# Kernel tuning notes

Hardware: AMD Instinct MI355X
Metric: run time of the kernel (lower is better)

## Reference

```python
import jax, jax.numpy as jnp
import numpy as np
import math

SIZE = 64
NLAND = 8
N_ITER = 6


def setup_inputs() -> dict:
    key = jax.random.key(0)
    k1, k2, k3 = jax.random.split(key, 3)
    B, T, C = 4, 4096, 1024
    return {
        "q": jax.random.normal(k1, (B, T, C), dtype=jnp.float32),
        "k": jax.random.normal(k2, (B, T, C), dtype=jnp.float32),
        "v": jax.random.normal(k3, (B, T, C), dtype=jnp.float32),
    }


def _iterative_pinv(mat, n_iter=N_ITER):
    # Newton-Schulz iteration for pseudo-inverse of [..., m, m] kernel.
    m = mat.shape[-1]
    I = jnp.eye(m, dtype=mat.dtype)
    K = mat
    # NOTE: torch.max over the whole tensor (global scalar), faithful to source.
    V = (1.0 / jnp.max(jnp.sum(K, axis=-2))) * jnp.swapaxes(K, -1, -2)
    for _ in range(n_iter):
        KV = jnp.matmul(K, V)
        V = jnp.matmul(0.25 * V, 13.0 * I - jnp.matmul(KV, 15.0 * I - jnp.matmul(KV, 7.0 * I - KV)))
    return V


def reference(q, k, v):
    B, T, C = q.shape
    H = C // SIZE
    scale = 1.0 / math.sqrt(SIZE)
    # Faithful reshape (not transpose) as in the source module.
    qh = q.reshape(B, H, T, SIZE)
    kh = k.reshape(B, H, T, SIZE)
    vh = v.reshape(B, H, T, SIZE)
    # T % NLAND == 0 branch: landmark = segment mean over T//NLAND tokens.
    q_l = qh.reshape(B, H, NLAND, T // NLAND, SIZE).mean(axis=-2)  # [B,H,m,d]
    k_l = kh.reshape(B, H, NLAND, T // NLAND, SIZE).mean(axis=-2)
    kernel_1 = jax.nn.softmax(jnp.einsum('bhtd,bhmd->bhtm', qh, k_l) * scale, axis=-1)  # [B,H,T,m]
    kernel_2 = jax.nn.softmax(jnp.einsum('bhmd,bhnd->bhmn', q_l, k_l) * scale, axis=-1)  # [B,H,m,m]
    kernel_3 = jax.nn.softmax(jnp.einsum('bhmd,bhtd->bhmt', q_l, kh) * scale, axis=-1)  # [B,H,m,T]
    pinv = _iterative_pinv(kernel_2)  # [B,H,m,m]
    k3v = jnp.matmul(kernel_3, vh)    # [B,H,m,d]
    out = jnp.matmul(jnp.matmul(kernel_1, pinv), k3v)  # [B,H,T,d]
    return out.reshape(B, T, C)
```

## Files before the change

### kernel.cpp

```cpp
#include <hip/hip_runtime.h>
#include <math.h>

#define T_TOK 4096
#define DD 64
#define NHEADS 64
#define SEG 512
#define SCALE 0.125f

#define QL_OFF   0
#define KL_OFF   32768
#define K2_OFF   65536
#define CS_OFF   69632
#define KP_OFF   70144
#define PA_OFF   332288
#define PD_OFF   2429440
#define W2_OFF   2462208

#define WAVE_BAR() __builtin_amdgcn_wave_barrier()

__global__ __launch_bounds__(256) void qsum_kernel(
    const float* __restrict__ q, float* __restrict__ ws) {
  int tid = threadIdx.x;
  const float4* q4 = (const float4*)q + (size_t)blockIdx.x * 8192;
  float4 b[2][8];
#pragma unroll
  for (int i = 0; i < 8; ++i) b[0][i] = q4[i * 256 + tid];
  float4 a = make_float4(0.f, 0.f, 0.f, 0.f);
#pragma unroll
  for (int j = 0; j < 4; ++j) {
    if (j < 3) {
#pragma unroll
      for (int i = 0; i < 8; ++i)
        b[(j + 1) & 1][i] = q4[(j + 1) * 2048 + i * 256 + tid];
    }
#pragma unroll
    for (int i = 0; i < 8; ++i) {
      float4 x = b[j & 1][i];
      a.x += x.x; a.y += x.y; a.z += x.z; a.w += x.w;
    }
  }
  __shared__ float4 red[16][17];
  red[tid >> 4][tid & 15] = a;
  __syncthreads();
  if (tid < 16) {
    float4 s = make_float4(0.f, 0.f, 0.f, 0.f);
#pragma unroll
    for (int g = 0; g < 16; ++g) {
      float4 r = red[g][tid];
      s.x += r.x; s.y += r.y; s.z += r.z; s.w += r.w;
    }
    const float inv = 1.f / (float)SEG;
    s.x *= inv; s.y *= inv; s.z *= inv; s.w *= inv;
    ((float4*)(ws + QL_OFF))[blockIdx.x * 16 + tid] = s;
  }
}

__global__ __launch_bounds__(256) void kvpass_kernel(
    const float* __restrict__ k, const float* __restrict__ v,
    float* __restrict__ ws) {
  int tid = threadIdx.x;
  int w = tid >> 6, lane = tid & 63;
  int gw = blockIdx.x * 4 + w;
  int hb = gw >> 6;
  int t8 = lane >> 3, m8 = lane & 7;
  int r0 = lane >> 4;
  __shared__ float qls[8][68];
  __shared__ float pl_all[4][16][12];
  float (*pl)[12] = pl_all[w];

  if (tid < 128) {
    float4 x = ((const float4*)(ws + QL_OFF))[hb * 128 + tid];
    *(float4*)&qls[tid >> 4][(tid & 15) * 4] = x;
  }
  __syncthreads();

  size_t base4 = (size_t)gw * 1024;
  const float4* k4 = (const float4*)k + base4;
  const float4* v4 = (const float4*)v + base4;

  float4 acc0 = make_float4(0.f,0.f,0.f,0.f), acc1 = make_float4(0.f,0.f,0.f,0.f);
  float4 acc2 = make_float4(0.f,0.f,0.f,0.f), acc3 = make_float4(0.f,0.f,0.f,0.f);
  float4 acc4 = make_float4(0.f,0.f,0.f,0.f), acc5 = make_float4(0.f,0.f,0.f,0.f);
  float4 acc6 = make_float4(0.f,0.f,0.f,0.f), acc7 = make_float4(0.f,0.f,0.f,0.f);
  float4 ksa = make_float4(0.f,0.f,0.f,0.f), ksb = make_float4(0.f,0.f,0.f,0.f);
  float den0=0.f,den1=0.f,den2=0.f,den3=0.f,den4=0.f,den5=0.f,den6=0.f,den7=0.f;

#pragma unroll 1
  for (int tile = 0; tile < 4; ++tile) {
    float4 vb0 = v4[tile * 256 + lane];
    float4 vb1 = v4[tile * 256 + 64 + lane];
    float4 vb2 = v4[tile * 256 + 128 + lane];
    float4 vb3 = v4[tile * 256 + 192 + lane];
#pragma unroll
    for (int rep = 0; rep < 2; ++rep) {
      int t = rep * 8 + t8;
      float4 ka = k4[(tile * 16 + t) * 16 + m8 * 2];
      float4 kb = k4[(tile * 16 + t) * 16 + m8 * 2 + 1];
      ksa.x += ka.x; ksa.y += ka.y; ksa.z += ka.z; ksa.w += ka.w;
      ksb.x += kb.x; ksb.y += kb.y; ksb.z += kb.z; ksb.w += kb.w;
      float p[8];
#pragma unroll
      for (int j = 0; j < 8; ++j) {
        const float4* qr = (const float4*)&qls[j][m8 * 8];
        float4 qa = qr[0], qb = qr[1];
        float dp = ka.x*qa.x + ka.y*qa.y + ka.z*qa.z + ka.w*qa.w
                 + kb.x*qb.x + kb.y*qb.y + kb.z*qb.z + kb.w*qb.w;
        dp += __shfl_xor(dp, 1, 64);
        dp += __shfl_xor(dp, 2, 64);
        dp += __shfl_xor(dp, 4, 64);
        p[j] = __expf(dp * SCALE);
      }
      den0 += p[0]; den1 += p[1]; den2 += p[2]; den3 += p[3];
      den4 += p[4]; den5 += p[5]; den6 += p[6]; den7 += p[7];
      float4 lo = make_float4(p[0], p[1], p[2], p[3]);
      float4 hi = make_float4(p[4], p[5], p[6], p[7]);
      if (m8 == 0) *(float4*)&pl[t][0] = lo;
      if (m8 == 1) *(float4*)&pl[t][4] = hi;
    }
    WAVE_BAR();
#pragma unroll
    for (int i = 0; i < 4; ++i) {
      int t = i * 4 + r0;
      float4 plo = *(const float4*)&pl[t][0];
      float4 phi = *(const float4*)&pl[t][4];
      float4 vv = (i == 0) ? vb0 : (i == 1) ? vb1 : (i == 2) ? vb2 : vb3;
      acc0.x += plo.x*vv.x; acc0.y += plo.x*vv.y; acc0.z += plo.x*vv.z; acc0.w += plo.x*vv.w;
      acc1.x += plo.y*vv.x; acc1.y += plo.y*vv.y; acc1.z += plo.y*vv.z; acc1.w += plo.y*vv.w;
      acc2.x += plo.z*vv.x; acc2.y += plo.z*vv.y; acc2.z += plo.z*vv.z; acc2.w += plo.z*vv.w;
      acc3.x += plo.w*vv.x; acc3.y += plo.w*vv.y; acc3.z += plo.w*vv.z; acc3.w += plo.w*vv.w;
      acc4.x += phi.x*vv.x; acc4.y += phi.x*vv.y; acc4.z += phi.x*vv.z; acc4.w += phi.x*vv.w;
      acc5.x += phi.y*vv.x; acc5.y += phi.y*vv.y; acc5.z += phi.y*vv.z; acc5.w += phi.y*vv.w;
      acc6.x += phi.z*vv.x; acc6.y += phi.z*vv.y; acc6.z += phi.z*vv.z; acc6.w += phi.z*vv.w;
      acc7.x += phi.w*vv.x; acc7.y += phi.w*vv.y; acc7.z += phi.w*vv.z; acc7.w += phi.w*vv.w;
    }
    WAVE_BAR();
  }
  ksa.x += __shfl_xor(ksa.x, 8, 64); ksa.y += __shfl_xor(ksa.y, 8, 64);
  ksa.z += __shfl_xor(ksa.z, 8, 64); ksa.w += __shfl_xor(ksa.w, 8, 64);
  ksb.x += __shfl_xor(ksb.x, 8, 64); ksb.y += __shfl_xor(ksb.y, 8, 64);
  ksb.z += __shfl_xor(ksb.z, 8, 64); ksb.w += __shfl_xor(ksb.w, 8, 64);
  ksa.x += __shfl_xor(ksa.x, 16, 64); ksa.y += __shfl_xor(ksa.y, 16, 64);
  ksa.z += __shfl_xor(ksa.z, 16, 64); ksa.w += __shfl_xor(ksa.w, 16, 64);
  ksb.x += __shfl_xor(ksb.x, 16, 64); ksb.y += __shfl_xor(ksb.y, 16, 64);
  ksb.z += __shfl_xor(ksb.z, 16, 64); ksb.w += __shfl_xor(ksb.w, 16, 64);
  ksa.x += __shfl_xor(ksa.x, 32, 64); ksa.y += __shfl_xor(ksa.y, 32, 64);
  ksa.z += __shfl_xor(ksa.z, 32, 64); ksa.w += __shfl_xor(ksa.w, 32, 64);
  ksb.x += __shfl_xor(ksb.x, 32, 64); ksb.y += __shfl_xor(ksb.y, 32, 64);
  ksb.z += __shfl_xor(ksb.z, 32, 64); ksb.w += __shfl_xor(ksb.w, 32, 64);
  if (lane < 8) {
    ((float4*)(ws + KP_OFF))[gw * 16 + lane * 2] = ksa;
    ((float4*)(ws + KP_OFF))[gw * 16 + lane * 2 + 1] = ksb;
  }
  den0 += __shfl_xor(den0, 8, 64); den1 += __shfl_xor(den1, 8, 64);
  den2 += __shfl_xor(den2, 8, 64); den3 += __shfl_xor(den3, 8, 64);
  den4 += __shfl_xor(den4, 8, 64); den5 += __shfl_xor(den5, 8, 64);
  den6 += __shfl_xor(den6, 8, 64); den7 += __shfl_xor(den7, 8, 64);
  den0 += __shfl_xor(den0, 16, 64); den1 += __shfl_xor(den1, 16, 64);
  den2 += __shfl_xor(den2, 16, 64); den3 += __shfl_xor(den3, 16, 64);
  den4 += __shfl_xor(den4, 16, 64); den5 += __shfl_xor(den5, 16, 64);
  den6 += __shfl_xor(den6, 16, 64); den7 += __shfl_xor(den7, 16, 64);
  den0 += __shfl_xor(den0, 32, 64); den1 += __shfl_xor(den1, 32, 64);
  den2 += __shfl_xor(den2, 32, 64); den3 += __shfl_xor(den3, 32, 64);
  den4 += __shfl_xor(den4, 32, 64); den5 += __shfl_xor(den5, 32, 64);
  den6 += __shfl_xor(den6, 32, 64); den7 += __shfl_xor(den7, 32, 64);
  if (lane == 0) {
    *(float4*)&ws[PD_OFF + (size_t)gw * 8] = make_float4(den0, den1, den2, den3);
    *(float4*)&ws[PD_OFF + (size_t)gw * 8 + 4] = make_float4(den4, den5, den6, den7);
  }
#define ACC_RED(A) \
  A.x += __shfl_xor(A.x, 16, 64); A.y += __shfl_xor(A.y, 16, 64); \
  A.z += __shfl_xor(A.z, 16, 64); A.w += __shfl_xor(A.w, 16, 64); \
  A.x += __shfl_xor(A.x, 32, 64); A.y += __shfl_xor(A.y, 32, 64); \
  A.z += __shfl_xor(A.z, 32, 64); A.w += __shfl_xor(A.w, 32, 64);
  ACC_RED(acc0) ACC_RED(acc1) ACC_RED(acc2) ACC_RED(acc3)
  ACC_RED(acc4) ACC_RED(acc5) ACC_RED(acc6) ACC_RED(acc7)
#undef ACC_RED
  if (lane < 16) {
    float4* pa = (float4*)(ws + PA_OFF) + (size_t)gw * 128;
    pa[0 * 16 + lane] = acc0;
    pa[1 * 16 + lane] = acc1;
    pa[2 * 16 + lane] = acc2;
    pa[3 * 16 + lane] = acc3;
    pa[4 * 16 + lane] = acc4;
    pa[5 * 16 + lane] = acc5;
    pa[6 * 16 + lane] = acc6;
    pa[7 * 16 + lane] = acc7;
  }
}

__global__ __launch_bounds__(512) void prepk_kernel(float* __restrict__ ws) {
  int hb = blockIdx.x, tid = threadIdx.x;
  __shared__ float qls[8][68];
  __shared__ float kls[8][68];
  __shared__ float ee[8][9];
  int m = tid >> 6, d = tid & 63;
  float s = 0.f;
#pragma unroll
  for (int j = 0; j < 8; ++j)
    s += ws[KP_OFF + (size_t)(hb * 64 + m * 8 + j) * 64 + d];
  s *= (1.f / (float)SEG);
  kls[m][d] = s;
  ws[KL_OFF + hb * 512 + tid] = s;
  qls[m][d] = ws[QL_OFF + hb * 512 + tid];
  __syncthreads();
  if (tid < 64) {
    int i = tid >> 3, j = tid & 7;
    float dot = 0.f;
#pragma unroll
    for (int dd = 0; dd < 64; ++dd) dot += qls[i][dd] * kls[j][dd];
    ee[i][j] = __expf(dot * SCALE);
  }
  __syncthreads();
  if (tid < 64) {
    int i = tid >> 3, j = tid & 7;
    float ssum = 0.f;
#pragma unroll
    for (int jj = 0; jj < 8; ++jj) ssum += ee[i][jj];
    ws[K2_OFF + hb * 64 + tid] = ee[i][j] / ssum;
  }
  if (tid < 8) {
    float cs = 0.f;
    for (int ii = 0; ii < 8; ++ii) {
      float ssum = 0.f;
#pragma unroll
      for (int jj = 0; jj < 8; ++jj) ssum += ee[ii][jj];
      cs += ee[ii][tid] / ssum;
    }
    ws[CS_OFF + hb * 8 + tid] = cs;
  }
}

__global__ __launch_bounds__(512) void pinvw2_kernel(float* __restrict__ ws) {
  int hb = blockIdx.x, tid = threadIdx.x;
  __shared__ float k3vs[8][68];
  __shared__ float K[8][9], V[8][9], X[8][9], Y[8][9];
  __shared__ float smax;
  int m = tid >> 6, d = tid & 63;
  float s = 0.f, den = 0.f;
  for (int c = 0; c < 64; ++c) {
    s += ws[PA_OFF + (((size_t)hb * 64 + c) * 8 + m) * 64 + d];
    den += ws[PD_OFF + ((size_t)hb * 64 + c) * 8 + m];
  }
  k3vs[m][d] = s / den;
  if (tid < 64) {
    float mx = 0.f;
    for (int t = 0; t < 8; ++t) mx = fmaxf(mx, ws[CS_OFF + t * 64 + tid]);
    for (int off = 32; off; off >>= 1) mx = fmaxf(mx, __shfl_xor(mx, off, 64));
    if (tid == 0) smax = mx;
  }
  int i = (tid >> 3) & 7, j = tid & 7;
  if (tid < 64) K[i][j] = ws[K2_OFF + hb * 64 + tid];
  __syncthreads();
  if (tid < 64) V[i][j] = K[j][i] * (1.f / smax);
  __syncthreads();
  for (int it = 0; it < 6; ++it) {
    float x = 0.f;
    if (tid < 64) {
      for (int kk = 0; kk < 8; ++kk) x += K[i][kk] * V[kk][j];
      X[i][j] = x;
    }
    __syncthreads();
    float bm = 0.f;
    if (tid < 64) {
      for (int kk = 0; kk < 8; ++kk) bm += X[i][kk] * X[kk][j];
      bm = 7.f * x - bm;
      Y[i][j] = bm;
    }
    __syncthreads();
    float dm = 0.f;
    if (tid < 64) {
      for (int kk = 0; kk < 8; ++kk) dm += X[i][kk] * Y[kk][j];
      dm = 15.f * x - dm;
    }
    __syncthreads();
    if (tid < 64) Y[i][j] = dm;
    __syncthreads();
    float vd = 0.f;
    if (tid < 64) {
      for (int kk = 0; kk < 8; ++kk) vd += V[i][kk] * Y[kk][j];
      vd = 0.25f * (13.f * V[i][j] - vd);
    }
    __syncthreads();
    if (tid < 64) V[i][j] = vd;
    __syncthreads();
  }
  float o = 0.f;
#pragma unroll
  for (int jj = 0; jj < 8; ++jj) o += V[m][jj] * k3vs[jj][d];
  ws[W2_OFF + hb * 512 + tid] = o;
}

__global__ __launch_bounds__(256) void out_kernel(
    const float* __restrict__ q, float* __restrict__ out,
    const float* __restrict__ ws) {
  int tid = threadIdx.x;
  int w = tid >> 6, lane = tid & 63;
  int gw = blockIdx.x * 4 + w;
  int hb = gw >> 6;
  __shared__ float qt_all[4][16][68];
  __shared__ float pl_all[4][16][9];
  __shared__ float w2_all[4][8][68];
  float (*qt)[68] = qt_all[w];
  float (*pl)[9]  = pl_all[w];
  float (*w2)[68] = w2_all[w];

  int m = lane & 7;
  float4 klrow[16];
#pragma unroll
  for (int d4 = 0; d4 < 16; ++d4)
    klrow[d4] = ((const float4*)(ws + KL_OFF))[hb * 128 + m * 16 + d4];
#pragma unroll
  for (int i = 0; i < 2; ++i) {
    int f4 = i * 64 + lane;
    float4 y = ((const float4*)(ws + W2_OFF))[hb * 128 + f4];
    *(float4*)&w2[f4 >> 4][(f4 & 15) * 4] = y;
  }

  size_t base4 = (size_t)gw * 1024;
  const float4* q4 = (const float4*)q + base4;
  float4* o4 = (float4*)out + base4;
  float4 buf[2][4];
#pragma unroll
  for (int i = 0; i < 4; ++i) buf[0][i] = q4[i * 64 + lane];

#pragma unroll
  for (int tile = 0; tile < 4; ++tile) {
    int cur = tile & 1;
    if (tile < 3) {
#pragma unroll
      for (int i = 0; i < 4; ++i)
        buf[cur ^ 1][i] = q4[(tile + 1) * 256 + i * 64 + lane];
    }
#pragma unroll
    for (int i = 0; i < 4; ++i) {
      int f4 = i * 64 + lane;
      *(float4*)&qt[f4 >> 4][(f4 & 15) * 4] = buf[cur][i];
    }
    WAVE_BAR();
#pragma unroll
    for (int rep = 0; rep < 2; ++rep) {
      int t = rep * 8 + (lane >> 3);
      const float4* qr = (const float4*)&qt[t][0];
      float dot = 0.f;
#pragma unroll
      for (int d4 = 0; d4 < 16; ++d4) {
        float4 a = qr[d4];
        dot += a.x * klrow[d4].x + a.y * klrow[d4].y +
               a.z * klrow[d4].z + a.w * klrow[d4].w;
      }
      pl[t][m] = __expf(dot * SCALE);
    }
    WAVE_BAR();
#pragma unroll
    for (int i = 0; i < 4; ++i) {
      int t = i * 4 + (lane >> 4);
      int qd = lane & 15;
      float p0 = pl[t][0], p1 = pl[t][1], p2 = pl[t][2], p3 = pl[t][3];
      float p4 = pl[t][4], p5 = pl[t][5], p6 = pl[t][6], p7 = pl[t][7];
      float inv = 1.f / (p0 + p1 + p2 + p3 + p4 + p5 + p6 + p7);
      float4 acc = make_float4(0.f, 0.f, 0.f, 0.f);
      float pm[8] = {p0, p1, p2, p3, p4, p5, p6, p7};
#pragma unroll
      for (int m2 = 0; m2 < 8; ++m2) {
        float wgt = pm[m2] * inv;
        float4 wv = *(const float4*)&w2[m2][qd * 4];
        acc.x += wgt * wv.x; acc.y += wgt * wv.y;
        acc.z += wgt * wv.z; acc.w += wgt * wv.w;
      }
      o4[tile * 256 + i * 64 + lane] = acc;
    }
    WAVE_BAR();
  }
}

extern "C" void kernel_launch(void* const* d_in, const int* in_sizes, int n_in,
                              void* d_out, int out_size, void* d_ws, size_t ws_size,
                              hipStream_t stream) {
  const float* q = (const float*)d_in[0];
  const float* k = (const float*)d_in[1];
  const float* v = (const float*)d_in[2];
  float* out = (float*)d_out;
  float* ws = (float*)d_ws;

  qsum_kernel<<<512, 256, 0, stream>>>(q, ws);
  kvpass_kernel<<<1024, 256, 0, stream>>>(k, v, ws);
  prepk_kernel<<<NHEADS, 512, 0, stream>>>(ws);
  pinvw2_kernel<<<NHEADS, 512, 0, stream>>>(ws);
  out_kernel<<<1024, 256, 0, stream>>>(q, out, ws);
}
```

Baseline: 84.32 us.

## Halve per-wave token span in kvpass and combine wave pairs in LDS

The kvpass kernel now launches twice as many blocks, and each wave processes 32 tokens (2 tiles) instead of 64. This raises parallelism and memory-level concurrency across the GPU. Partial sums from pairs of waves are added in shared memory before being written, so the workspace layout and the number of partial records the downstream kernels read stay the same. The cost is an extra __syncthreads, some LDS traffic, and a per-wave epilogue of shuffle reductions that is now amortized over half as much work.

```diff
diff --git a/kernel.cpp b/kernel.cpp
--- a/kernel.cpp
+++ b/kernel.cpp
@@ -60,12 +60,13 @@
     float* __restrict__ ws) {
   int tid = threadIdx.x;
   int w = tid >> 6, lane = tid & 63;
-  int gw = blockIdx.x * 4 + w;
-  int hb = gw >> 6;
-  int t8 = lane >> 3, m8 = lane & 7;
-  int r0 = lane >> 4;
+  int hb = blockIdx.x >> 5;
+  int t8 = lane >> 3, m8 = lane & 7, r0 = lane >> 4;
   __shared__ float qls[8][68];
   __shared__ float pl_all[4][16][12];
+  __shared__ float4 accred[4][8][16];
+  __shared__ float4 ksred[4][16];
+  __shared__ float dens[4][8];
   float (*pl)[12] = pl_all[w];
 
   if (tid < 128) {
@@ -74,9 +75,9 @@
   }
   __syncthreads();
 
-  size_t base4 = (size_t)gw * 1024;
-  const float4* k4 = (const float4*)k + base4;
-  const float4* v4 = (const float4*)v + base4;
+  size_t tok0 = (size_t)blockIdx.x * 128 + (size_t)w * 32;
+  const float4* k4 = (const float4*)k + tok0 * 16;
+  const float4* v4 = (const float4*)v + tok0 * 16;
 
   float4 acc0 = make_float4(0.f,0.f,0.f,0.f), acc1 = make_float4(0.f,0.f,0.f,0.f);
   float4 acc2 = make_float4(0.f,0.f,0.f,0.f), acc3 = make_float4(0.f,0.f,0.f,0.f);
@@ -86,7 +87,7 @@
   float den0=0.f,den1=0.f,den2=0.f,den3=0.f,den4=0.f,den5=0.f,den6=0.f,den7=0.f;
 
 #pragma unroll 1
-  for (int tile = 0; tile < 4; ++tile) {
+  for (int tile = 0; tile < 2; ++tile) {
     float4 vb0 = v4[tile * 256 + lane];
     float4 vb1 = v4[tile * 256 + 64 + lane];
     float4 vb2 = v4[tile * 256 + 128 + lane];
@@ -148,8 +149,8 @@
   ksb.x += __shfl_xor(ksb.x, 32, 64); ksb.y += __shfl_xor(ksb.y, 32, 64);
   ksb.z += __shfl_xor(ksb.z, 32, 64); ksb.w += __shfl_xor(ksb.w, 32, 64);
   if (lane < 8) {
-    ((float4*)(ws + KP_OFF))[gw * 16 + lane * 2] = ksa;
-    ((float4*)(ws + KP_OFF))[gw * 16 + lane * 2 + 1] = ksb;
+    ksred[w][lane * 2] = ksa;
+    ksred[w][lane * 2 + 1] = ksb;
   }
   den0 += __shfl_xor(den0, 8, 64); den1 += __shfl_xor(den1, 8, 64);
   den2 += __shfl_xor(den2, 8, 64); den3 += __shfl_xor(den3, 8, 64);
@@ -164,8 +165,8 @@
   den4 += __shfl_xor(den4, 32, 64); den5 += __shfl_xor(den5, 32, 64);
   den6 += __shfl_xor(den6, 32, 64); den7 += __shfl_xor(den7, 32, 64);
   if (lane == 0) {
-    *(float4*)&ws[PD_OFF + (size_t)gw * 8] = make_float4(den0, den1, den2, den3);
-    *(float4*)&ws[PD_OFF + (size_t)gw * 8 + 4] = make_float4(den4, den5, den6, den7);
+    *(float4*)&dens[w][0] = make_float4(den0, den1, den2, den3);
+    *(float4*)&dens[w][4] = make_float4(den4, den5, den6, den7);
   }
 #define ACC_RED(A) \
   A.x += __shfl_xor(A.x, 16, 64); A.y += __shfl_xor(A.y, 16, 64); \
@@ -176,16 +177,33 @@
   ACC_RED(acc4) ACC_RED(acc5) ACC_RED(acc6) ACC_RED(acc7)
 #undef ACC_RED
   if (lane < 16) {
-    float4* pa = (float4*)(ws + PA_OFF) + (size_t)gw * 128;
-    pa[0 * 16 + lane] = acc0;
-    pa[1 * 16 + lane] = acc1;
-    pa[2 * 16 + lane] = acc2;
-    pa[3 * 16 + lane] = acc3;
-    pa[4 * 16 + lane] = acc4;
-    pa[5 * 16 + lane] = acc5;
-    pa[6 * 16 + lane] = acc6;
-    pa[7 * 16 + lane] = acc7;
-  }
+    accred[w][0][lane] = acc0;
+    accred[w][1][lane] = acc1;
+    accred[w][2][lane] = acc2;
+    accred[w][3][lane] = acc3;
+    accred[w][4][lane] = acc4;
+    accred[w][5][lane] = acc5;
+    accred[w][6][lane] = acc6;
+    accred[w][7][lane] = acc7;
+  }
+  __syncthreads();
+  int half = tid >> 7;
+  int gwc = blockIdx.x * 2 + half;
+  int w0 = half * 2, w1 = w0 + 1;
+  int li = tid & 127;
+  {
+    int mm = li >> 4, d4 = li & 15;
+    float4 a = accred[w0][mm][d4], b = accred[w1][mm][d4];
+    float4 s = make_float4(a.x + b.x, a.y + b.y, a.z + b.z, a.w + b.w);
+    ((float4*)(ws + PA_OFF))[((size_t)gwc * 8 + mm) * 16 + d4] = s;
+  }
+  if (li < 16) {
+    float4 a = ksred[w0][li], b = ksred[w1][li];
+    float4 s = make_float4(a.x + b.x, a.y + b.y, a.z + b.z, a.w + b.w);
+    ((float4*)(ws + KP_OFF))[gwc * 16 + li] = s;
+  }
+  if (li < 8)
+    ws[PD_OFF + (size_t)gwc * 8 + li] = dens[w0][li] + dens[w1][li];
 }
 
 __global__ __launch_bounds__(512) void prepk_kernel(float* __restrict__ ws) {
@@ -383,7 +401,7 @@
   float* ws = (float*)d_ws;
 
   qsum_kernel<<<512, 256, 0, stream>>>(q, ws);
-  kvpass_kernel<<<1024, 256, 0, stream>>>(k, v, ws);
+  kvpass_kernel<<<2048, 256, 0, stream>>>(k, v, ws);
   prepk_kernel<<<NHEADS, 512, 0, stream>>>(ws);
   pinvw2_kernel<<<NHEADS, 512, 0, stream>>>(ws);
   out_kernel<<<1024, 256, 0, stream>>>(q, out, ws);
```

After: 89.39 us. 1.06x slower.
